# Optimization experiments

Measured on AMD Instinct MI355X. Metric: run time of the kernel, lower is better.

The kernel has to match this reference:

```python
import jax, jax.numpy as jnp
import numpy as np

BATCH, N_AGENTS, OBS_DIM, ACTOR_DIM, N_ACTIONS = 8192, 64, 128, 64, 32


def setup_inputs() -> dict:
    key = jax.random.key(0)
    ks = jax.random.split(key, 14)
    s = 0.05
    inp = {
        "O": jax.random.normal(ks[0], (BATCH, N_AGENTS, OBS_DIM), dtype=jnp.float32),
        "W_enc": jax.random.normal(ks[1], (OBS_DIM, ACTOR_DIM), dtype=jnp.float32) * s,
        "b_enc": jax.random.normal(ks[2], (ACTOR_DIM,), dtype=jnp.float32) * s,
        "W1": jax.random.normal(ks[3], (2 * ACTOR_DIM, ACTOR_DIM), dtype=jnp.float32) * s,
        "b1": jax.random.normal(ks[4], (ACTOR_DIM,), dtype=jnp.float32) * s,
        "W2": jax.random.normal(ks[5], (2 * ACTOR_DIM, ACTOR_DIM), dtype=jnp.float32) * s,
        "b2": jax.random.normal(ks[6], (ACTOR_DIM,), dtype=jnp.float32) * s,
        "W3": jax.random.normal(ks[7], (2 * ACTOR_DIM, ACTOR_DIM), dtype=jnp.float32) * s,
        "b3": jax.random.normal(ks[8], (ACTOR_DIM,), dtype=jnp.float32) * s,
        "W4": jax.random.normal(ks[9], (2 * ACTOR_DIM, ACTOR_DIM), dtype=jnp.float32) * s,
        "b4": jax.random.normal(ks[10], (ACTOR_DIM,), dtype=jnp.float32) * s,
        "W_dec": jax.random.normal(ks[11], (N_AGENTS * ACTOR_DIM, N_ACTIONS), dtype=jnp.float32) * s,
        "b_dec": jax.random.normal(ks[12], (N_ACTIONS,), dtype=jnp.float32) * s,
    }
    return inp


def _comm_layer(H, W, b, n_agents):
    # get_commvar: masked mean over other agents, but divided by n_agents
    # (the zeroed self term is included in the mean denominator) ->
    # C_i = (sum_j H_j - H_i) / n_agents, exactly equal to the original math.
    C = (jnp.sum(H, axis=1, keepdims=True) - H) / n_agents  # [B, A, D]
    Hcat = jnp.concatenate([H, C], axis=-1)                 # [B, A, 2D]
    return Hcat @ W + b                                     # no activation (faithful)


def reference(O, W_enc, b_enc, W1, b1, W2, b2, W3, b3, W4, b4, W_dec, b_dec):
    B, A, _ = O.shape
    H = jax.nn.sigmoid(O @ W_enc + b_enc)  # [B, A, D]
    H = _comm_layer(H, W1, b1, A)
    H = _comm_layer(H, W2, b2, A)
    H = _comm_layer(H, W3, b3, A)
    H = _comm_layer(H, W4, b4, A)
    Hf = H.reshape(B, -1)                  # [B, A*D]
    return Hf @ W_dec + b_dec              # [B, n_actions]
```

## Files before the change

kernel.cpp:

```cpp
#include <hip/hip_runtime.h>
#include <stdint.h>


#define BATCHN 8192
#define NAGENT 64
#define OBSD   128
#define DD     64
#define NACT   32

typedef __attribute__((ext_vector_type(8))) short short8;
typedef __attribute__((ext_vector_type(4))) float floatx4;

__device__ __forceinline__ unsigned short f2b(float f) {
    union { float f; uint32_t u; } v; v.f = f;
    uint32_t r = v.u + 0x7FFFu + ((v.u >> 16) & 1u);
    return (unsigned short)(r >> 16);
}

#define OFF_WENC 0
#define OFF_WCAT 16384
#define OFF_WDEC 81920
#define OFF_H4   344064

__global__ __launch_bounds__(256) void prep_kernel(
    const float* __restrict__ Wenc,
    const float* __restrict__ W1, const float* __restrict__ W2,
    const float* __restrict__ W3, const float* __restrict__ W4,
    const float* __restrict__ Wdec,
    unsigned short* __restrict__ ws)
{
    int tid = blockIdx.x * 256 + threadIdx.x;
    if (tid < 8192) {
        int n = tid >> 7, k = tid & 127;
        ws[OFF_WENC/2 + n*128 + k] = f2b(Wenc[k*64 + n]);
    } else if (tid < 5*8192) {
        int l = (tid - 8192) >> 13;
        int e = (tid - 8192) & 8191;
        int n = e >> 7, k = e & 127;
        const float* W = (l==0) ? W1 : (l==1) ? W2 : (l==2) ? W3 : W4;
        float v = W[k*64 + n];
        if (k < 64) v -= W[(k+64)*64 + n] * (1.0f/64.0f);
        ws[OFF_WCAT/2 + l*8192 + n*128 + k] = f2b(v);
    } else {
        int e = tid - 5*8192;
        int n = e >> 12, k = e & 4095;
        ws[OFF_WDEC/2 + n*4096 + k] = f2b(Wdec[k*32 + n]);
    }
}

__global__ __launch_bounds__(256) void fused_kernel(
    const float* __restrict__ O,
    const unsigned short* __restrict__ WencT,
    const unsigned short* __restrict__ WcatT,
    const float* __restrict__ b_enc,
    const float* __restrict__ b1, const float* __restrict__ b2,
    const float* __restrict__ b3, const float* __restrict__ b4,
    unsigned short* __restrict__ H4out)
{
    __shared__ __align__(16) unsigned short sA[64*136];
    __shared__ __align__(16) unsigned short sW[64*136];
    __shared__ __align__(16) unsigned short sH[64*72];
    __shared__ __align__(16) unsigned short sS[64];
    __shared__ float sPart[4][64];

    const int t = threadIdx.x;
    const int b = blockIdx.x;
    const int lane = t & 63;
    const int w = t >> 6;
    const int m = lane & 15;
    const int q = lane >> 4;

    {
        const float* Ob = O + (size_t)b * (NAGENT*OBSD);
        #pragma unroll
        for (int i = 0; i < 8; i++) {
            int e = t*4 + i*1024;
            float4 f = *(const float4*)(Ob + e);
            int row = e >> 7, col = e & 127;
            uint2 pk;
            pk.x = (uint32_t)f2b(f.x) | ((uint32_t)f2b(f.y) << 16);
            pk.y = (uint32_t)f2b(f.z) | ((uint32_t)f2b(f.w) << 16);
            *(uint2*)&sA[row*136 + col] = pk;
        }
        #pragma unroll
        for (int i = 0; i < 4; i++) {
            int c = t + i*256;
            int e = c*8;
            int row = e >> 7, col = e & 127;
            *(uint4*)&sW[row*136 + col] = *(const uint4*)(WencT + e);
        }
    }
    __syncthreads();

    floatx4 acc[4];

    #pragma unroll
    for (int nt = 0; nt < 4; nt++) {
        float bias = b_enc[nt*16 + m];
        acc[nt] = (floatx4){bias, bias, bias, bias};
    }
    #pragma unroll
    for (int s = 0; s < 4; s++) {
        short8 a = *(const short8*)&sA[(w*16 + m)*136 + s*32 + q*8];
        #pragma unroll
        for (int nt = 0; nt < 4; nt++) {
            short8 bb = *(const short8*)&sW[(nt*16 + m)*136 + s*32 + q*8];
            acc[nt] = __builtin_amdgcn_mfma_f32_16x16x32_bf16(a, bb, acc[nt], 0, 0, 0);
        }
    }
    #pragma unroll
    for (int nt = 0; nt < 4; nt++)
        #pragma unroll
        for (int r = 0; r < 4; r++)
            acc[nt][r] = 1.0f / (1.0f + __expf(-acc[nt][r]));

    #pragma unroll
    for (int nt = 0; nt < 4; nt++) {
        float s = acc[nt][0] + acc[nt][1] + acc[nt][2] + acc[nt][3];
        s += __shfl_xor(s, 16, 64);
        s += __shfl_xor(s, 32, 64);
        if (q == 0) sPart[w][nt*16 + m] = s;
        #pragma unroll
        for (int r = 0; r < 4; r++)
            sH[(w*16 + q*4 + r)*72 + nt*16 + m] = f2b(acc[nt][r]);
    }

    const float* bs[4] = {b1, b2, b3, b4};
    #pragma unroll
    for (int l = 0; l < 4; l++) {
        __syncthreads();
        #pragma unroll
        for (int i = 0; i < 4; i++) {
            int c = t + i*256;
            int e = c*8;
            int row = e >> 7, col = e & 127;
            *(uint4*)&sW[row*136 + col] = *(const uint4*)(WcatT + l*8192 + e);
        }
        if (t < 64)
            sS[t] = f2b((sPart[0][t] + sPart[1][t] + sPart[2][t] + sPart[3][t]) * (1.0f/64.0f));
        __syncthreads();

        const float* bl = bs[l];
        #pragma unroll
        for (int nt = 0; nt < 4; nt++) {
            float bias = bl[nt*16 + m];
            acc[nt] = (floatx4){bias, bias, bias, bias};
        }
        #pragma unroll
        for (int s = 0; s < 2; s++) {
            short8 a = *(const short8*)&sH[(w*16 + m)*72 + s*32 + q*8];
            #pragma unroll
            for (int nt = 0; nt < 4; nt++) {
                short8 bb = *(const short8*)&sW[(nt*16 + m)*136 + s*32 + q*8];
                acc[nt] = __builtin_amdgcn_mfma_f32_16x16x32_bf16(a, bb, acc[nt], 0, 0, 0);
            }
        }
        #pragma unroll
        for (int s = 0; s < 2; s++) {
            short8 a = *(const short8*)&sS[s*32 + q*8];
            #pragma unroll
            for (int nt = 0; nt < 4; nt++) {
                short8 bb = *(const short8*)&sW[(nt*16 + m)*136 + (s+2)*32 + q*8];
                acc[nt] = __builtin_amdgcn_mfma_f32_16x16x32_bf16(a, bb, acc[nt], 0, 0, 0);
            }
        }

        if (l < 3) {
            #pragma unroll
            for (int nt = 0; nt < 4; nt++) {
                float s = acc[nt][0] + acc[nt][1] + acc[nt][2] + acc[nt][3];
                s += __shfl_xor(s, 16, 64);
                s += __shfl_xor(s, 32, 64);
                if (q == 0) sPart[w][nt*16 + m] = s;
                #pragma unroll
                for (int r = 0; r < 4; r++)
                    sH[(w*16 + q*4 + r)*72 + nt*16 + m] = f2b(acc[nt][r]);
            }
        } else {
            unsigned short* Hb = H4out + (size_t)b * 4096;
            #pragma unroll
            for (int nt = 0; nt < 4; nt++)
                #pragma unroll
                for (int r = 0; r < 4; r++)
                    Hb[(w*16 + q*4 + r)*64 + nt*16 + m] = f2b(acc[nt][r]);
        }
    }
}

__global__ __launch_bounds__(256) void dec_kernel(
    const unsigned short* __restrict__ Hf,
    const unsigned short* __restrict__ WdecT,
    const float* __restrict__ b_dec,
    float* __restrict__ out)
{
    int gt = blockIdx.x * 256 + threadIdx.x;
    int wave = gt >> 6;
    int lane = gt & 63;
    int rb = wave >> 3;
    int kc = wave & 7;
    int m = lane & 15, q = lane >> 4;

    const unsigned short* aP  = Hf    + (size_t)(rb*16 + m)*4096 + kc*512 + q*8;
    const unsigned short* bP0 = WdecT + (size_t)m*4096        + kc*512 + q*8;
    const unsigned short* bP1 = WdecT + (size_t)(16 + m)*4096 + kc*512 + q*8;

    floatx4 a0 = {0.f, 0.f, 0.f, 0.f}, a1 = {0.f, 0.f, 0.f, 0.f};
    #pragma unroll 4
    for (int s = 0; s < 16; s++) {
        short8 av  = *(const short8*)(aP  + s*32);
        short8 b0v = *(const short8*)(bP0 + s*32);
        short8 b1v = *(const short8*)(bP1 + s*32);
        a0 = __builtin_amdgcn_mfma_f32_16x16x32_bf16(av, b0v, a0, 0, 0, 0);
        a1 = __builtin_amdgcn_mfma_f32_16x16x32_bf16(av, b1v, a1, 0, 0, 0);
    }
    float bias0 = (kc == 0) ? b_dec[m]      : 0.0f;
    float bias1 = (kc == 0) ? b_dec[16 + m] : 0.0f;
    #pragma unroll
    for (int r = 0; r < 4; r++) {
        int row = rb*16 + q*4 + r;
        atomicAdd(&out[row*32 + m],      a0[r] + bias0);
        atomicAdd(&out[row*32 + 16 + m], a1[r] + bias1);
    }
}

extern "C" void kernel_launch(void* const* d_in, const int* in_sizes, int n_in,
                              void* d_out, int out_size, void* d_ws, size_t ws_size,
                              hipStream_t stream)
{
    const float* O    = (const float*)d_in[0];
    const float* Wenc = (const float*)d_in[1];
    const float* benc = (const float*)d_in[2];
    const float* W1   = (const float*)d_in[3];
    const float* b1   = (const float*)d_in[4];
    const float* W2   = (const float*)d_in[5];
    const float* b2   = (const float*)d_in[6];
    const float* W3   = (const float*)d_in[7];
    const float* b3   = (const float*)d_in[8];
    const float* W4   = (const float*)d_in[9];
    const float* b4   = (const float*)d_in[10];
    const float* Wdec = (const float*)d_in[11];
    const float* bdec = (const float*)d_in[12];
    float* out = (float*)d_out;
    unsigned short* ws = (unsigned short*)d_ws;

    hipMemsetAsync(d_out, 0, (size_t)out_size * sizeof(float), stream);
    prep_kernel<<<672, 256, 0, stream>>>(Wenc, W1, W2, W3, W4, Wdec, ws);
    fused_kernel<<<BATCHN, 256, 0, stream>>>(O, ws + OFF_WENC/2, ws + OFF_WCAT/2,
                                             benc, b1, b2, b3, b4, ws + OFF_H4/2);
    dec_kernel<<<1024, 256, 0, stream>>>(ws + OFF_H4/2, ws + OFF_WDEC/2, bdec, out);
}
```

Measured before the change: 453.7 us.

## Process one batch element per wave with register-resident weights, no block barriers

Each wave now owns an entire batch element (64 agents × 64 dims as a 4×4 MFMA tile grid). It reads O directly from global memory into registers and keeps the weight fragments in registers loaded straight from global, so the LDS staging of O and weights and all __syncthreads go away. Per-wave LDS holds only the H and mean buffers, the agent-mean reduction becomes wave-local, and bf16 packing uses the paired conversion intrinsic. In exchange the kernel uses much more register space (64 accumulator floats plus 16 weight fragments), declares 2 blocks per SM, and has four times fewer blocks. Each wave also repeats the weight loads from global/L2.

```diff
diff --git a/kernel.cpp b/kernel.cpp
--- a/kernel.cpp
+++ b/kernel.cpp
@@ -1,12 +1,9 @@
 #include <hip/hip_runtime.h>
+#include <hip/hip_bf16.h>
 #include <stdint.h>
 
 
 #define BATCHN 8192
-#define NAGENT 64
-#define OBSD   128
-#define DD     64
-#define NACT   32
 
 typedef __attribute__((ext_vector_type(8))) short short8;
 typedef __attribute__((ext_vector_type(4))) float floatx4;
@@ -15,6 +12,13 @@
     union { float f; uint32_t u; } v; v.f = f;
     uint32_t r = v.u + 0x7FFFu + ((v.u >> 16) & 1u);
     return (unsigned short)(r >> 16);
+}
+
+__device__ __forceinline__ uint32_t pk2(float x, float y) {
+    float2 t; t.x = x; t.y = y;
+    __hip_bfloat162 h = __float22bfloat162_rn(t);
+    union { __hip_bfloat162 h; uint32_t u; } c; c.h = h;
+    return c.u;
 }
 
 #define OFF_WENC 0
@@ -48,7 +52,7 @@
     }
 }
 
-__global__ __launch_bounds__(256) void fused_kernel(
+__global__ __launch_bounds__(256, 2) void fused2_kernel(
     const float* __restrict__ O,
     const unsigned short* __restrict__ WencT,
     const unsigned short* __restrict__ WcatT,
@@ -57,134 +61,141 @@
     const float* __restrict__ b3, const float* __restrict__ b4,
     unsigned short* __restrict__ H4out)
 {
-    __shared__ __align__(16) unsigned short sA[64*136];
-    __shared__ __align__(16) unsigned short sW[64*136];
-    __shared__ __align__(16) unsigned short sH[64*72];
-    __shared__ __align__(16) unsigned short sS[64];
-    __shared__ float sPart[4][64];
-
-    const int t = threadIdx.x;
-    const int b = blockIdx.x;
-    const int lane = t & 63;
-    const int w = t >> 6;
-    const int m = lane & 15;
-    const int q = lane >> 4;
-
+    __shared__ unsigned short sH[4][64*72];
+    __shared__ unsigned short sS[4][72];
+
+    const int t = threadIdx.x, lane = t & 63, w = t >> 6;
+    const int m = lane & 15, q = lane >> 4;
+    const int b = blockIdx.x * 4 + w;
+    unsigned short* myH = sH[w];
+    unsigned short* myS = sS[w];
+
+    float bias[5][4];
     {
-        const float* Ob = O + (size_t)b * (NAGENT*OBSD);
-        #pragma unroll
-        for (int i = 0; i < 8; i++) {
-            int e = t*4 + i*1024;
-            float4 f = *(const float4*)(Ob + e);
-            int row = e >> 7, col = e & 127;
-            uint2 pk;
-            pk.x = (uint32_t)f2b(f.x) | ((uint32_t)f2b(f.y) << 16);
-            pk.y = (uint32_t)f2b(f.z) | ((uint32_t)f2b(f.w) << 16);
-            *(uint2*)&sA[row*136 + col] = pk;
-        }
-        #pragma unroll
-        for (int i = 0; i < 4; i++) {
-            int c = t + i*256;
-            int e = c*8;
-            int row = e >> 7, col = e & 127;
-            *(uint4*)&sW[row*136 + col] = *(const uint4*)(WencT + e);
-        }
-    }
-    __syncthreads();
-
-    floatx4 acc[4];
-
-    #pragma unroll
-    for (int nt = 0; nt < 4; nt++) {
-        float bias = b_enc[nt*16 + m];
-        acc[nt] = (floatx4){bias, bias, bias, bias};
-    }
+        const float* bp[5] = {b_enc, b1, b2, b3, b4};
+        #pragma unroll
+        for (int l = 0; l < 5; l++)
+            #pragma unroll
+            for (int nt = 0; nt < 4; nt++)
+                bias[l][nt] = bp[l][nt*16 + m];
+    }
+
+    floatx4 acc[4][4];
+    short8  Bf[16];
+
+    #pragma unroll
+    for (int nt = 0; nt < 4; nt++)
+        #pragma unroll
+        for (int s = 0; s < 4; s++)
+            Bf[nt*4+s] = *(const short8*)(WencT + (nt*16+m)*128 + s*32 + q*8);
+
+    #pragma unroll
+    for (int mt = 0; mt < 4; mt++)
+        #pragma unroll
+        for (int nt = 0; nt < 4; nt++)
+            acc[mt][nt] = (floatx4){bias[0][nt], bias[0][nt], bias[0][nt], bias[0][nt]};
+
+    const float* Ob = O + (size_t)b * 8192;
     #pragma unroll
     for (int s = 0; s < 4; s++) {
-        short8 a = *(const short8*)&sA[(w*16 + m)*136 + s*32 + q*8];
+        short8 A[4];
+        #pragma unroll
+        for (int mt = 0; mt < 4; mt++) {
+            const float* pr = Ob + (mt*16+m)*128 + s*32 + q*8;
+            float4 f0 = *(const float4*)pr;
+            float4 f1 = *(const float4*)(pr + 4);
+            uint32_t* pa = (uint32_t*)&A[mt];
+            pa[0] = pk2(f0.x, f0.y); pa[1] = pk2(f0.z, f0.w);
+            pa[2] = pk2(f1.x, f1.y); pa[3] = pk2(f1.z, f1.w);
+        }
+        #pragma unroll
+        for (int mt = 0; mt < 4; mt++)
+            #pragma unroll
+            for (int nt = 0; nt < 4; nt++)
+                acc[mt][nt] = __builtin_amdgcn_mfma_f32_16x16x32_bf16(A[mt], Bf[nt*4+s], acc[mt][nt], 0, 0, 0);
+    }
+    #pragma unroll
+    for (int mt = 0; mt < 4; mt++)
+        #pragma unroll
+        for (int nt = 0; nt < 4; nt++)
+            #pragma unroll
+            for (int r = 0; r < 4; r++)
+                acc[mt][nt][r] = 1.0f / (1.0f + __expf(-acc[mt][nt][r]));
+
+    #pragma unroll
+    for (int l = 1; l <= 4; l++) {
         #pragma unroll
         for (int nt = 0; nt < 4; nt++) {
-            short8 bb = *(const short8*)&sW[(nt*16 + m)*136 + s*32 + q*8];
-            acc[nt] = __builtin_amdgcn_mfma_f32_16x16x32_bf16(a, bb, acc[nt], 0, 0, 0);
-        }
-    }
-    #pragma unroll
-    for (int nt = 0; nt < 4; nt++)
-        #pragma unroll
-        for (int r = 0; r < 4; r++)
-            acc[nt][r] = 1.0f / (1.0f + __expf(-acc[nt][r]));
-
-    #pragma unroll
-    for (int nt = 0; nt < 4; nt++) {
-        float s = acc[nt][0] + acc[nt][1] + acc[nt][2] + acc[nt][3];
-        s += __shfl_xor(s, 16, 64);
-        s += __shfl_xor(s, 32, 64);
-        if (q == 0) sPart[w][nt*16 + m] = s;
-        #pragma unroll
-        for (int r = 0; r < 4; r++)
-            sH[(w*16 + q*4 + r)*72 + nt*16 + m] = f2b(acc[nt][r]);
-    }
-
-    const float* bs[4] = {b1, b2, b3, b4};
-    #pragma unroll
-    for (int l = 0; l < 4; l++) {
-        __syncthreads();
-        #pragma unroll
-        for (int i = 0; i < 4; i++) {
-            int c = t + i*256;
-            int e = c*8;
-            int row = e >> 7, col = e & 127;
-            *(uint4*)&sW[row*136 + col] = *(const uint4*)(WcatT + l*8192 + e);
-        }
-        if (t < 64)
-            sS[t] = f2b((sPart[0][t] + sPart[1][t] + sPart[2][t] + sPart[3][t]) * (1.0f/64.0f));
-        __syncthreads();
-
-        const float* bl = bs[l];
+            float s = 0.f;
+            #pragma unroll
+            for (int mt = 0; mt < 4; mt++)
+                #pragma unroll
+                for (int r = 0; r < 4; r++) s += acc[mt][nt][r];
+            s += __shfl_xor(s, 16, 64);
+            s += __shfl_xor(s, 32, 64);
+            if (q == 0) myS[nt*16 + m] = f2b(s * (1.0f/64.0f));
+        }
+        #pragma unroll
+        for (int mt = 0; mt < 4; mt++)
+            #pragma unroll
+            for (int nt = 0; nt < 4; nt++) {
+                uint32_t p01 = pk2(acc[mt][nt][0], acc[mt][nt][1]);
+                uint32_t p23 = pk2(acc[mt][nt][2], acc[mt][nt][3]);
+                unsigned short* base = myH + (mt*16 + q*4)*72 + nt*16 + m;
+                base[0]   = (unsigned short)p01;
+                base[72]  = (unsigned short)(p01 >> 16);
+                base[144] = (unsigned short)p23;
+                base[216] = (unsigned short)(p23 >> 16);
+            }
+
+        #pragma unroll
+        for (int nt = 0; nt < 4; nt++)
+            #pragma unroll
+            for (int s = 0; s < 4; s++)
+                Bf[nt*4+s] = *(const short8*)(WcatT + (l-1)*8192 + (nt*16+m)*128 + s*32 + q*8);
+
+        #pragma unroll
+        for (int mt = 0; mt < 4; mt++)
+            #pragma unroll
+            for (int nt = 0; nt < 4; nt++)
+                acc[mt][nt] = (floatx4){bias[l][nt], bias[l][nt], bias[l][nt], bias[l][nt]};
+
+        #pragma unroll
+        for (int s2 = 0; s2 < 2; s2++) {
+            short8 A[4];
+            #pragma unroll
+            for (int mt = 0; mt < 4; mt++)
+                A[mt] = *(const short8*)(myH + (mt*16+m)*72 + s2*32 + q*8);
+            #pragma unroll
+            for (int mt = 0; mt < 4; mt++)
+                #pragma unroll
+                for (int nt = 0; nt < 4; nt++)
+                    acc[mt][nt] = __builtin_amdgcn_mfma_f32_16x16x32_bf16(A[mt], Bf[nt*4+s2], acc[mt][nt], 0, 0, 0);
+        }
+        #pragma unroll
+        for (int s2 = 0; s2 < 2; s2++) {
+            short8 As = *(const short8*)(myS + s2*32 + q*8);
+            #pragma unroll
+            for (int mt = 0; mt < 4; mt++)
+                #pragma unroll
+                for (int nt = 0; nt < 4; nt++)
+                    acc[mt][nt] = __builtin_amdgcn_mfma_f32_16x16x32_bf16(As, Bf[nt*4+2+s2], acc[mt][nt], 0, 0, 0);
+        }
+    }
+
+    unsigned short* Hb = H4out + (size_t)b * 4096;
+    #pragma unroll
+    for (int mt = 0; mt < 4; mt++)
         #pragma unroll
         for (int nt = 0; nt < 4; nt++) {
-            float bias = bl[nt*16 + m];
-            acc[nt] = (floatx4){bias, bias, bias, bias};
-        }
-        #pragma unroll
-        for (int s = 0; s < 2; s++) {
-            short8 a = *(const short8*)&sH[(w*16 + m)*72 + s*32 + q*8];
-            #pragma unroll
-            for (int nt = 0; nt < 4; nt++) {
-                short8 bb = *(const short8*)&sW[(nt*16 + m)*136 + s*32 + q*8];
-                acc[nt] = __builtin_amdgcn_mfma_f32_16x16x32_bf16(a, bb, acc[nt], 0, 0, 0);
-            }
-        }
-        #pragma unroll
-        for (int s = 0; s < 2; s++) {
-            short8 a = *(const short8*)&sS[s*32 + q*8];
-            #pragma unroll
-            for (int nt = 0; nt < 4; nt++) {
-                short8 bb = *(const short8*)&sW[(nt*16 + m)*136 + (s+2)*32 + q*8];
-                acc[nt] = __builtin_amdgcn_mfma_f32_16x16x32_bf16(a, bb, acc[nt], 0, 0, 0);
-            }
-        }
-
-        if (l < 3) {
-            #pragma unroll
-            for (int nt = 0; nt < 4; nt++) {
-                float s = acc[nt][0] + acc[nt][1] + acc[nt][2] + acc[nt][3];
-                s += __shfl_xor(s, 16, 64);
-                s += __shfl_xor(s, 32, 64);
-                if (q == 0) sPart[w][nt*16 + m] = s;
-                #pragma unroll
-                for (int r = 0; r < 4; r++)
-                    sH[(w*16 + q*4 + r)*72 + nt*16 + m] = f2b(acc[nt][r]);
-            }
-        } else {
-            unsigned short* Hb = H4out + (size_t)b * 4096;
-            #pragma unroll
-            for (int nt = 0; nt < 4; nt++)
-                #pragma unroll
-                for (int r = 0; r < 4; r++)
-                    Hb[(w*16 + q*4 + r)*64 + nt*16 + m] = f2b(acc[nt][r]);
-        }
-    }
+            uint32_t p01 = pk2(acc[mt][nt][0], acc[mt][nt][1]);
+            uint32_t p23 = pk2(acc[mt][nt][2], acc[mt][nt][3]);
+            unsigned short* base = Hb + (mt*16 + q*4)*64 + nt*16 + m;
+            base[0]   = (unsigned short)p01;
+            base[64]  = (unsigned short)(p01 >> 16);
+            base[128] = (unsigned short)p23;
+            base[192] = (unsigned short)(p23 >> 16);
+        }
 }
 
 __global__ __launch_bounds__(256) void dec_kernel(
@@ -245,7 +256,7 @@
 
     hipMemsetAsync(d_out, 0, (size_t)out_size * sizeof(float), stream);
     prep_kernel<<<672, 256, 0, stream>>>(Wenc, W1, W2, W3, W4, Wdec, ws);
-    fused_kernel<<<BATCHN, 256, 0, stream>>>(O, ws + OFF_WENC/2, ws + OFF_WCAT/2,
-                                             benc, b1, b2, b3, b4, ws + OFF_H4/2);
+    fused2_kernel<<<2048, 256, 0, stream>>>(O, ws + OFF_WENC/2, ws + OFF_WCAT/2,
+                                            benc, b1, b2, b3, b4, ws + OFF_H4/2);
     dec_kernel<<<1024, 256, 0, stream>>>(ws + OFF_H4/2, ws + OFF_WDEC/2, bdec, out);
 }
```

Result: slower. 474.1 us (+4.5%).
